# Kernel optimization log

Hardware: AMD Instinct MI355X
Metric: run time of the kernel (lower is better)

## Reference

```python
import jax, jax.numpy as jnp
import numpy as np

N = 30000      # nodes
E = 480000     # edges
NF = 92        # node features
EF = 50        # edge features
D1 = 64        # dim1
D2 = 64        # dim2
L = 3          # conv_count
FC = 2         # fc_count
G = 256        # graphs in batch
EPS = 1e-5


def setup_inputs() -> dict:
    key = jax.random.key(0)
    ks = jax.random.split(key, 20)
    s = 0.05
    zd = 2 * D1 + EF  # CGConv concat dim
    inp = {
        "x": jax.random.normal(ks[0], (N, NF), jnp.float32),
        "edge_attr": jax.random.uniform(ks[1], (E, EF), jnp.float32),
        "lin0_w": jax.random.normal(ks[2], (NF, D1), jnp.float32) * s,
        "lin0_b": jnp.zeros((D1,), jnp.float32),
        "conv_wf": jax.random.normal(ks[3], (L, zd, D1), jnp.float32) * s,
        "conv_bf": jnp.zeros((L, D1), jnp.float32),
        "conv_ws": jax.random.normal(ks[4], (L, zd, D1), jnp.float32) * s,
        "conv_bs": jnp.zeros((L, D1), jnp.float32),
        "bn_gamma": jnp.ones((L, D1), jnp.float32),
        "bn_beta": jnp.zeros((L, D1), jnp.float32),
        "lin1_w": jax.random.normal(ks[5], (D1, D2), jnp.float32) * s,
        "lin1_b": jnp.zeros((D2,), jnp.float32),
        "fc_w": jax.random.normal(ks[6], (FC, D2, D2), jnp.float32) * s,
        "fc_b": jnp.zeros((FC, D2), jnp.float32),
        "lin2_w": jax.random.normal(ks[7], (D2, 1), jnp.float32) * s,
        "lin2_b": jnp.zeros((1,), jnp.float32),
        "edge_index": jax.random.randint(ks[8], (2, E), 0, N),
        "batch": jnp.sort(jax.random.randint(ks[9], (N,), 0, G)),
        "n_graphs": G,
    }
    return inp


def reference(x, edge_attr, lin0_w, lin0_b, conv_wf, conv_bf, conv_ws, conv_bs,
              bn_gamma, bn_beta, lin1_w, lin1_b, fc_w, fc_b, lin2_w, lin2_b,
              edge_index, batch, n_graphs):
    n = x.shape[0]
    src = edge_index[0]  # x_j (source)
    dst = edge_index[1]  # x_i (target, aggregation index)
    h = jax.nn.relu(x @ lin0_w + lin0_b)  # [N, D1]

    # per-target edge counts for mean aggregation (constant across layers)
    cnt = jax.ops.segment_sum(jnp.ones((src.shape[0],), h.dtype), dst, num_segments=n)
    cnt = jnp.maximum(cnt, 1.0)[:, None]

    for l in range(L):
        # z = [x_i || x_j || e_ij]  -> gated message sigmoid(Wf z) * softplus(Ws z)
        z = jnp.concatenate([h[dst], h[src], edge_attr], axis=-1)  # [E, 2*D1+EF]
        m = jax.nn.sigmoid(z @ conv_wf[l] + conv_bf[l]) * jax.nn.softplus(z @ conv_ws[l] + conv_bs[l])
        aggr = jax.ops.segment_sum(m, dst, num_segments=n) / cnt  # mean aggr [N, D1]
        # BatchNorm (training-mode batch stats, biased variance as in torch)
        mu = jnp.mean(aggr, axis=0)
        var = jnp.var(aggr, axis=0)
        aggr = (aggr - mu) * jax.lax.rsqrt(var + EPS) * bn_gamma[l] + bn_beta[l]
        h = jax.nn.relu(h + aggr)  # residual then outer ReLU

    # global mean pool over graphs
    gcnt = jnp.maximum(jax.ops.segment_sum(jnp.ones((n,), h.dtype), batch, num_segments=n_graphs), 1.0)[:, None]
    out = jax.ops.segment_sum(h, batch, num_segments=n_graphs) / gcnt  # [G, D1]

    out = jax.nn.relu(out @ lin1_w + lin1_b)
    for f in range(FC):
        out = jax.nn.relu(out @ fc_w[f] + fc_b[f])
    out = out @ lin2_w + lin2_b
    return out.reshape(-1)  # [G]
```

## Files before the change

kernel.cpp:

```cpp
#include <hip/hip_runtime.h>
#include <hip/hip_bf16.h>

#define N_NODES 30000
#define N_EDGES 480000
#define NFEAT 92
#define EFEAT 50
#define D1 64
#define ZD 178
#define NL 3
#define NG 256
#define BN_EPS 1e-5f
#define NTILES (N_EDGES / 16)
#define EDGE_BLOCKS 7500
#define EDGE_GRID 7504

#define LIN0_BLOCKS 512
#define CNT_BLOCKS 1875
#define WPREP_BLOCKS 96
#define SCAN_BLOCKS ((N_NODES + 255) / 256)
#define BUILD_BLOCKS 1875
#define NP_BLOCKS 1024

typedef __attribute__((ext_vector_type(8))) short bf16x8;
typedef __attribute__((ext_vector_type(8))) unsigned short u16x8;
typedef __attribute__((ext_vector_type(4))) unsigned short u16x4;
typedef __attribute__((ext_vector_type(4))) float f32x4;

static __device__ __forceinline__ unsigned short f2bf(float v) {
  __hip_bfloat16 b = __float2bfloat16(v);
  return *(unsigned short*)&b;
}
static __device__ __forceinline__ float bfu(unsigned short u) {
  union { unsigned int i; float f; } c;
  c.i = ((unsigned int)u) << 16;
  return c.f;
}

static __device__ __forceinline__ void nodeproj_body(
    int blk0, int nblk, const float* __restrict__ hin, float* __restrict__ hout,
    const float* __restrict__ wfp, const float* __restrict__ wsm,
    unsigned short* __restrict__ projd_pk, unsigned short* __restrict__ projs_pk,
    const float* __restrict__ aggr, float* __restrict__ aggr_z,
    const float* __restrict__ invc, const float* __restrict__ musum,
    const float* __restrict__ sqsum, const float* __restrict__ gamma,
    const float* __restrict__ beta, int do_bn, float (*hl)[64]) {
  const int lane = threadIdx.x & 63;
  const int w = threadIdx.x >> 6;
  const float* W = (w < 2) ? wfp : wsm;
  const int roff = (w & 1) * 64;
  float wreg[D1];
#pragma unroll
  for (int k = 0; k < D1; ++k) wreg[k] = W[(size_t)(roff + k) * D1 + lane];
  unsigned short* pk = (w & 1) ? projs_pk : projd_pk;
  const int slot = (w < 2) ? 0 : 4;
  const int poff = (lane >> 2) * 8 + (lane & 3) + slot;
  float r = 0.0f, sh = 0.0f;
  if (do_bn) {
    const float mu = musum[lane] * (1.0f / N_NODES);
    const float var = sqsum[lane] * (1.0f / N_NODES) - mu * mu;
    r = gamma[lane] * rsqrtf(var + BN_EPS);
    sh = beta[lane] - mu * r;
  }
  for (int i = blk0; i < N_NODES; i += nblk) {
    float hv = hin[(size_t)i * D1 + lane];
    if (do_bn) {
      const float av = aggr[(size_t)i * D1 + lane] * invc[i];
      hv = fmaxf(hv + fmaf(av, r, sh), 0.0f);
      if (w == 0) hout[(size_t)i * D1 + lane] = hv;
    }
    if (w == 1) aggr_z[(size_t)i * D1 + lane] = 0.0f;
    hl[w][lane] = hv;
    __builtin_amdgcn_wave_barrier();
    const float4* hr = (const float4*)&hl[w][0];
    float acc = 0.0f;
#pragma unroll
    for (int k4 = 0; k4 < D1 / 4; ++k4) {
      const float4 v = hr[k4];
      acc = fmaf(v.x, wreg[4 * k4 + 0], acc);
      acc = fmaf(v.y, wreg[4 * k4 + 1], acc);
      acc = fmaf(v.z, wreg[4 * k4 + 2], acc);
      acc = fmaf(v.w, wreg[4 * k4 + 3], acc);
    }
    pk[(size_t)i * 128 + poff] = f2bf(acc);
    __builtin_amdgcn_wave_barrier();
  }
}

extern "C" __global__ void __launch_bounds__(256)
k_init(const float* __restrict__ x, const float* __restrict__ w,
       const float* __restrict__ b, float* __restrict__ h,
       const int* __restrict__ ei, int* __restrict__ cnt,
       const float* __restrict__ conv_wf, const float* __restrict__ conv_ws,
       unsigned short* __restrict__ Bp) {
  const int blk = blockIdx.x;
  if (blk < LIN0_BLOCKS) {
    const int lane = threadIdx.x & 63;
    const int wave = (blk * 256 + threadIdx.x) >> 6;
    const int nw = (LIN0_BLOCKS * 256) >> 6;
    float wreg[NFEAT];
#pragma unroll
    for (int k = 0; k < NFEAT; ++k) wreg[k] = w[k * D1 + lane];
    const float bj = b[lane];
    for (int i = wave; i < N_NODES; i += nw) {
      const float2* xr = (const float2*)(x + (size_t)i * NFEAT);
      float acc = bj;
#pragma unroll
      for (int k = 0; k < NFEAT / 2; ++k) {
        const float2 v = xr[k];
        acc = fmaf(v.x, wreg[2 * k], acc);
        acc = fmaf(v.y, wreg[2 * k + 1], acc);
      }
      h[(size_t)i * D1 + lane] = fmaxf(acc, 0.0f);
    }
  } else if (blk < LIN0_BLOCKS + CNT_BLOCKS) {
    const int e = (blk - LIN0_BLOCKS) * 256 + threadIdx.x;
    if (e < N_EDGES) atomicAdd(&cnt[ei[N_EDGES + e]], 1);
  } else {
    const int idx = (blk - LIN0_BLOCKS - CNT_BLOCKS) * 256 + threadIdx.x;
    const int j = idx & 7;
    const int lane = (idx >> 3) & 63;
    const int frag = (idx >> 9) & 15;
    const int l = idx >> 13;
    const int n = frag & 3;
    const int t = (frag >> 2) & 1;
    const int m = frag >> 3;
    const int k = t * 32 + (lane >> 4) * 8 + j;
    const int feat = (lane & 15) * 4 + n;
    float v = 0.0f;
    if (k < EFEAT) {
      const float* W = (m == 0) ? conv_wf : conv_ws;
      v = W[(size_t)l * ZD * D1 + (size_t)(128 + k) * D1 + feat];
    }
    Bp[idx] = f2bf(v);
  }
}

extern "C" __global__ void __launch_bounds__(256)
k_scan1(const int* __restrict__ cnt, int* __restrict__ lpre, int* __restrict__ ptot) {
  const int t = threadIdx.x;
  const int idx = blockIdx.x * 256 + t;
  const int v = (idx < N_NODES) ? cnt[idx] : 0;
  __shared__ int bs[256];
  bs[t] = v;
  __syncthreads();
  for (int off = 1; off < 256; off <<= 1) {
    int u = (t >= off) ? bs[t - off] : 0;
    __syncthreads();
    bs[t] += u;
    __syncthreads();
  }
  if (idx < N_NODES) lpre[idx] = bs[t] - v;
  if (t == 255) ptot[blockIdx.x] = bs[255];
}

extern "C" __global__ void __launch_bounds__(256)
k_scan23(const int* __restrict__ cnt, const int* __restrict__ lpre,
         const int* __restrict__ ptot, const int* __restrict__ batch,
         int* __restrict__ wptr, float* __restrict__ invc,
         int* __restrict__ grp) {
  __shared__ int bs[128];
  const int t = threadIdx.x;
  if (t < 128) bs[t] = (t < SCAN_BLOCKS) ? ptot[t] : 0;
  __syncthreads();
  for (int off = 1; off < 128; off <<= 1) {
    int u = 0;
    if (t < 128 && t >= off) u = bs[t - off];
    __syncthreads();
    if (t < 128 && t >= off) bs[t] += u;
    __syncthreads();
  }
  const int idx = blockIdx.x * 256 + t;
  if (idx >= N_NODES) return;
  const int bid = idx >> 8;
  const int boff = (bid == 0) ? 0 : bs[bid - 1];
  wptr[idx] = boff + lpre[idx];
  invc[idx] = 1.0f / fmaxf((float)cnt[idx], 1.0f);
  const int bt = batch[idx];
  if (idx == 0)
    for (int g = 0; g <= bt; ++g) grp[g] = 0;
  else {
    const int pb = batch[idx - 1];
    for (int g = pb + 1; g <= bt; ++g) grp[g] = idx;
  }
  if (idx == N_NODES - 1)
    for (int g = bt + 1; g <= NG; ++g) grp[g] = N_NODES;
}

extern "C" __global__ void __launch_bounds__(256)
k_build(const int* __restrict__ ei, int* __restrict__ wptr,
        int2* __restrict__ ds2, const float* __restrict__ ea,
        unsigned short* __restrict__ eapb,
        const float* __restrict__ h0, const float* __restrict__ wfl,
        const float* __restrict__ wsl, unsigned short* __restrict__ projd_pk,
        unsigned short* __restrict__ projs_pk, float* __restrict__ aggrA) {
  __shared__ __align__(16) int lpos[256];
  if (blockIdx.x >= BUILD_BLOCKS) {
    nodeproj_body(blockIdx.x - BUILD_BLOCKS, NP_BLOCKS, h0, nullptr, wfl, wsl,
                  projd_pk, projs_pk, nullptr, aggrA, nullptr, nullptr, nullptr,
                  nullptr, nullptr, 0, (float(*)[64])lpos);
    return;
  }
  const int e0 = blockIdx.x * 256;
  {
    const int e = e0 + threadIdx.x;
    const int d = ei[N_EDGES + e];
    const int pos = atomicAdd(&wptr[d], 1);
    ds2[pos] = make_int2(d, ei[e]);
    lpos[threadIdx.x] = pos;
  }
  __syncthreads();
  const int l16 = threadIdx.x & 15;
  const int sub = threadIdx.x >> 4;
#pragma unroll
  for (int r = 0; r < 16; ++r) {
    const int eb = r * 16 + sub;
    const size_t ge = e0 + eb;
    const int pos = lpos[eb];
    unsigned short o0 = 0, o1 = 0, o2 = 0, o3 = 0;
    if (l16 < 12) {
      const float4 v = *(const float4*)(ea + ge * EFEAT + l16 * 4);
      o0 = f2bf(v.x); o1 = f2bf(v.y); o2 = f2bf(v.z); o3 = f2bf(v.w);
    } else if (l16 == 12) {
      const float2 v = *(const float2*)(ea + ge * EFEAT + 48);
      o0 = f2bf(v.x); o1 = f2bf(v.y);
    }
    u16x4 st;
    st[0] = o0; st[1] = o1; st[2] = o2; st[3] = o3;
    *(u16x4*)(eapb + ((size_t)pos << 6) + l16 * 4) = st;
  }
}

extern "C" __global__ void __launch_bounds__(256)
k_nodeproj(const float* __restrict__ hin, float* __restrict__ hout,
           const float* __restrict__ wfp, const float* __restrict__ wsm,
           unsigned short* __restrict__ projd_pk, unsigned short* __restrict__ projs_pk,
           const float* __restrict__ aggr, float* __restrict__ aggr_z,
           const float* __restrict__ invc,
           const float* __restrict__ musum, const float* __restrict__ sqsum,
           const float* __restrict__ gamma, const float* __restrict__ beta) {
  __shared__ float hl[4][64];
  nodeproj_body(blockIdx.x, gridDim.x, hin, hout, wfp, wsm, projd_pk, projs_pk,
                aggr, aggr_z, invc, musum, sqsum, gamma, beta, 1, hl);
}

extern "C" __global__ void __launch_bounds__(256)
k_edgemm(const unsigned short* __restrict__ projd_pk,
         const unsigned short* __restrict__ projs_pk,
         const unsigned short* __restrict__ eapb,
         const int2* __restrict__ ds2,
         const unsigned short* __restrict__ Bp,
         const float* __restrict__ bfp, const float* __restrict__ bsp,
         float* __restrict__ aggr, float* __restrict__ musum,
         float* __restrict__ sqsum) {
  const int lane = threadIdx.x & 63;
  const int wv = threadIdx.x >> 6;
  const int col = lane & 15;
  const int quad = lane >> 4;
  __shared__ float mlds[4][16][68];

  const int vbid = (blockIdx.x & 7) * 938 + (blockIdx.x >> 3);
  if (blockIdx.x == 0 && wv == 0) {
    musum[lane] = 0.0f;
    sqsum[lane] = 0.0f;
  }
  if (vbid >= EDGE_BLOCKS) return;

  const int t = vbid * 4 + wv;
  const int base = t * 16;

  const int4 p01 = *(const int4*)(ds2 + base + quad * 4);
  const int4 p23 = *(const int4*)(ds2 + base + quad * 4 + 2);
  const int dr[4] = {p01.x, p01.z, p23.x, p23.z};
  const int sr[4] = {p01.y, p01.w, p23.y, p23.w};
  const bf16x8 Af0 = *(const bf16x8*)(eapb + ((size_t)(base + col) << 6) + quad * 8);
  const bf16x8 Af1 = *(const bf16x8*)(eapb + ((size_t)(base + col) << 6) + 32 + quad * 8);

  bf16x8 Bf[2][2][4];
#pragma unroll
  for (int m = 0; m < 2; ++m)
#pragma unroll
    for (int tt = 0; tt < 2; ++tt)
#pragma unroll
      for (int n = 0; n < 4; ++n)
        Bf[m][tt][n] = *(const bf16x8*)(Bp + ((((m * 2 + tt) * 4 + n) * 64 + lane) * 8));

  const f32x4 bf4 = *(const f32x4*)(bfp + col * 4);
  const f32x4 bs4 = *(const f32x4*)(bsp + col * 4);

  f32x4 aF[4], aS[4];
#pragma unroll
  for (int r = 0; r < 4; ++r) {
    const int d = dr[r];
    const int s = sr[r];
    const u16x8 pd = *(const u16x8*)(projd_pk + (size_t)d * 128 + col * 8);
    const u16x8 ss = *(const u16x8*)(projs_pk + (size_t)s * 128 + col * 8);
#pragma unroll
    for (int n = 0; n < 4; ++n) {
      aF[n][r] = bfu(pd[n]) + bfu(ss[n]) + bf4[n];
      aS[n][r] = bfu(pd[n + 4]) + bfu(ss[n + 4]) + bs4[n];
    }
  }

#pragma unroll
  for (int n = 0; n < 4; ++n) {
    aF[n] = __builtin_amdgcn_mfma_f32_16x16x32_bf16(Af0, Bf[0][0][n], aF[n], 0, 0, 0);
    aF[n] = __builtin_amdgcn_mfma_f32_16x16x32_bf16(Af1, Bf[0][1][n], aF[n], 0, 0, 0);
    aS[n] = __builtin_amdgcn_mfma_f32_16x16x32_bf16(Af0, Bf[1][0][n], aS[n], 0, 0, 0);
    aS[n] = __builtin_amdgcn_mfma_f32_16x16x32_bf16(Af1, Bf[1][1][n], aS[n], 0, 0, 0);
  }

#pragma unroll
  for (int r = 0; r < 4; ++r) {
    f32x4 mv;
#pragma unroll
    for (int n = 0; n < 4; ++n) {
      const float af = aF[n][r];
      const float as = aS[n][r];
      const float sg = __builtin_amdgcn_rcpf(1.0f + __expf(-af));
      const float sp = fmaxf(as, 0.0f) + __logf(1.0f + __expf(-fabsf(as)));
      mv[n] = sg * sp;
    }
    *(f32x4*)&mlds[wv][quad * 4 + r][col * 4] = mv;
  }
  __builtin_amdgcn_wave_barrier();

  float sum = 0.0f;
  int dcur = ds2[base].x;
#pragma unroll
  for (int p = 0; p < 16; ++p) {
    sum += mlds[wv][p][lane];
    const int dnxt = (p < 15) ? ds2[base + p + 1].x : -1;
    if (dnxt != dcur) {
      atomicAdd(&aggr[(size_t)dcur * D1 + lane], sum);
      sum = 0.0f;
      dcur = dnxt;
    }
  }
}

extern "C" __global__ void __launch_bounds__(256)
k_stats(const float* __restrict__ aggr, const float* __restrict__ invc,
        float* __restrict__ musum, float* __restrict__ sqsum) {
  const int j = threadIdx.x & 63;
  const int rid = (blockIdx.x * blockDim.x + threadIdx.x) >> 6;
  const int rstr = (gridDim.x * blockDim.x) >> 6;
  float s = 0.0f, sq = 0.0f;
  for (int i = rid; i < N_NODES; i += rstr) {
    const float v = aggr[(size_t)i * D1 + j] * invc[i];
    s += v;
    sq = fmaf(v, v, sq);
  }
  __shared__ float ls[256], lq[256];
  ls[threadIdx.x] = s;
  lq[threadIdx.x] = sq;
  __syncthreads();
  if (threadIdx.x < 64) {
    s = ls[j] + ls[64 + j] + ls[128 + j] + ls[192 + j];
    sq = lq[j] + lq[64 + j] + lq[128 + j] + lq[192 + j];
    atomicAdd(&musum[j], s);
    atomicAdd(&sqsum[j], sq);
  }
}

extern "C" __global__ void __launch_bounds__(256)
k_poolmlp(const float* __restrict__ h, const float* __restrict__ aggr,
          const float* __restrict__ invc,
          const float* __restrict__ musum, const float* __restrict__ sqsum,
          const float* __restrict__ gamma, const float* __restrict__ beta,
          const int* __restrict__ grp,
          const float* __restrict__ lin1_w, const float* __restrict__ lin1_b,
          const float* __restrict__ fc_w, const float* __restrict__ fc_b,
          const float* __restrict__ lin2_w, const float* __restrict__ lin2_b,
          float* __restrict__ out) {
  const int g = blockIdx.x;
  const int lane = threadIdx.x & 63;
  const int wv = threadIdx.x >> 6;
  const float mu = musum[lane] * (1.0f / N_NODES);
  const float var = sqsum[lane] * (1.0f / N_NODES) - mu * mu;
  const float r = gamma[lane] * rsqrtf(var + BN_EPS);
  const float sh = beta[lane] - mu * r;
  const int s = grp[g], e = grp[g + 1];
  float acc = 0.0f;
  for (int i = s + wv; i < e; i += 4) {
    const float hv = h[(size_t)i * D1 + lane];
    const float av = aggr[(size_t)i * D1 + lane] * invc[i];
    acc += fmaxf(hv + fmaf(av, r, sh), 0.0f);
  }
  __shared__ float red[4][64];
  __shared__ float vin[64];
  red[wv][lane] = acc;
  __syncthreads();
  const int j = threadIdx.x;
  float v = 0.0f;
  if (j < 64) {
    const float inv = 1.0f / fmaxf((float)(e - s), 1.0f);
    v = (red[0][j] + red[1][j] + red[2][j] + red[3][j]) * inv;
  }
  for (int layer = 0; layer < 3; ++layer) {
    if (j < 64) vin[j] = v;
    __syncthreads();
    if (j < 64) {
      const float* W;
      const float* B;
      if (layer == 0) {
        W = lin1_w;
        B = lin1_b;
      } else {
        W = fc_w + (size_t)(layer - 1) * D1 * D1;
        B = fc_b + (size_t)(layer - 1) * D1;
      }
      float a2 = B[j];
#pragma unroll 16
      for (int k = 0; k < D1; ++k) a2 = fmaf(vin[k], W[k * D1 + j], a2);
      v = fmaxf(a2, 0.0f);
    }
    __syncthreads();
  }
  if (j < 64) {
    float p = v * lin2_w[j];
#pragma unroll
    for (int off = 32; off > 0; off >>= 1) p += __shfl_down(p, off);
    if (j == 0) out[g] = p + lin2_b[0];
  }
}

extern "C" void kernel_launch(void* const* d_in, const int* in_sizes, int n_in,
                              void* d_out, int out_size, void* d_ws, size_t ws_size,
                              hipStream_t stream) {
  const float* x        = (const float*)d_in[0];
  const float* ea       = (const float*)d_in[1];
  const float* lin0_w   = (const float*)d_in[2];
  const float* lin0_b   = (const float*)d_in[3];
  const float* conv_wf  = (const float*)d_in[4];
  const float* conv_bf  = (const float*)d_in[5];
  const float* conv_ws  = (const float*)d_in[6];
  const float* conv_bs  = (const float*)d_in[7];
  const float* bn_gamma = (const float*)d_in[8];
  const float* bn_beta  = (const float*)d_in[9];
  const float* lin1_w   = (const float*)d_in[10];
  const float* lin1_b   = (const float*)d_in[11];
  const float* fc_w     = (const float*)d_in[12];
  const float* fc_b     = (const float*)d_in[13];
  const float* lin2_w   = (const float*)d_in[14];
  const float* lin2_b   = (const float*)d_in[15];
  const int*   ei       = (const int*)d_in[16];
  const int*   batch    = (const int*)d_in[17];

  uintptr_t p = (uintptr_t)d_ws;
  auto alloc = [&](size_t bytes) {
    p = (p + 255) & ~(size_t)255;
    void* r = (void*)p;
    p += bytes;
    return r;
  };
  float* h0     = (float*)alloc((size_t)N_NODES * 64 * 4);
  float* h1     = (float*)alloc((size_t)N_NODES * 64 * 4);
  unsigned short* projd_pk = (unsigned short*)alloc((size_t)N_NODES * 128 * 2);
  unsigned short* projs_pk = (unsigned short*)alloc((size_t)N_NODES * 128 * 2);
  float* aggrA  = (float*)alloc((size_t)N_NODES * 64 * 4);
  float* aggrB  = (float*)alloc((size_t)N_NODES * 64 * 4);
  float* musum  = (float*)alloc(128 * 4);
  float* sqsum  = musum + 64;
  float* invc   = (float*)alloc((size_t)N_NODES * 4);
  int*   cnt    = (int*)alloc((size_t)N_NODES * 4);
  int*   lpre   = (int*)alloc((size_t)N_NODES * 4);
  int*   ptot   = (int*)alloc((size_t)SCAN_BLOCKS * 4);
  int*   wptr   = (int*)alloc((size_t)N_NODES * 4);
  int2*  ds2    = (int2*)alloc((size_t)N_EDGES * 8);
  int*   grp    = (int*)alloc((size_t)(NG + 1) * 4);
  unsigned short* eapb = (unsigned short*)alloc((size_t)N_EDGES * 64 * 2);
  unsigned short* Bp   = (unsigned short*)alloc((size_t)NL * 16 * 64 * 8 * 2);

  hipMemsetAsync(cnt, 0, N_NODES * sizeof(int), stream);
  k_init<<<LIN0_BLOCKS + CNT_BLOCKS + WPREP_BLOCKS, 256, 0, stream>>>(
      x, lin0_w, lin0_b, h0, ei, cnt, conv_wf, conv_ws, Bp);
  k_scan1<<<SCAN_BLOCKS, 256, 0, stream>>>(cnt, lpre, ptot);
  k_scan23<<<SCAN_BLOCKS, 256, 0, stream>>>(cnt, lpre, ptot, batch, wptr, invc, grp);
  k_build<<<BUILD_BLOCKS + NP_BLOCKS, 256, 0, stream>>>(
      ei, wptr, ds2, ea, eapb, h0, conv_wf, conv_ws, projd_pk, projs_pk, aggrA);

  float* aggr_of[NL] = {aggrA, aggrB, aggrA};
  const float* hin_of[NL]  = {h0, h0, h1};
  float* hout_of[NL]       = {h0, h1, h0};

  for (int l = 0; l < NL; ++l) {
    const float* wfl = conv_wf + (size_t)l * ZD * D1;
    const float* wsl = conv_ws + (size_t)l * ZD * D1;
    if (l > 0)
      k_nodeproj<<<1024, 256, 0, stream>>>(
          hin_of[l], hout_of[l], wfl, wsl, projd_pk, projs_pk,
          aggr_of[l - 1], aggr_of[l], invc, musum, sqsum,
          bn_gamma + (size_t)(l - 1) * D1, bn_beta + (size_t)(l - 1) * D1);
    k_edgemm<<<EDGE_GRID, 256, 0, stream>>>(
        projd_pk, projs_pk, eapb, ds2,
        Bp + (size_t)l * 16 * 64 * 8,
        conv_bf + (size_t)l * D1, conv_bs + (size_t)l * D1,
        aggr_of[l], musum, sqsum);
    k_stats<<<256, 256, 0, stream>>>(aggr_of[l], invc, musum, sqsum);
  }

  k_poolmlp<<<NG, 256, 0, stream>>>(h0, aggr_of[2], invc, musum, sqsum,
                                    bn_gamma + (size_t)2 * D1, bn_beta + (size_t)2 * D1,
                                    grp, lin1_w, lin1_b, fc_w, fc_b,
                                    lin2_w, lin2_b, (float*)d_out);
}
```

Before: 621.7 us.

## Fuse whole pipeline into one cooperative persistent kernel with grid syncs

Replaces the sequence of separate kernel launches (init, scans, build, per-layer nodeproj/edge/stats, pool) with a single cooperative kernel of 1024 persistent blocks. The phases are separated by grid.sync, and the edge loop is grid-strided instead of one tile per block. Per-layer BN statistics now get separate buffers and are zeroed up front. This removes launch gaps and tail effects between the many small kernels. The cost is grid-wide barrier overhead, lower occupancy from __launch_bounds__(256,4) and fewer blocks on the edge phase. A fallback multi-kernel path is kept for devices without cooperative launch.

```diff
diff --git a/kernel.cpp b/kernel.cpp
--- a/kernel.cpp
+++ b/kernel.cpp
@@ -1,5 +1,8 @@
 #include <hip/hip_runtime.h>
 #include <hip/hip_bf16.h>
+#include <hip/hip_cooperative_groups.h>
+
+namespace cg = cooperative_groups;
 
 #define N_NODES 30000
 #define N_EDGES 480000
@@ -11,20 +14,25 @@
 #define NG 256
 #define BN_EPS 1e-5f
 #define NTILES (N_EDGES / 16)
-#define EDGE_BLOCKS 7500
-#define EDGE_GRID 7504
-
-#define LIN0_BLOCKS 512
-#define CNT_BLOCKS 1875
-#define WPREP_BLOCKS 96
 #define SCAN_BLOCKS ((N_NODES + 255) / 256)
-#define BUILD_BLOCKS 1875
-#define NP_BLOCKS 1024
+#define BUILD_CHUNKS 1875
+#define NB 1024
+#define SMEM_BYTES 17408
 
 typedef __attribute__((ext_vector_type(8))) short bf16x8;
 typedef __attribute__((ext_vector_type(8))) unsigned short u16x8;
 typedef __attribute__((ext_vector_type(4))) unsigned short u16x4;
 typedef __attribute__((ext_vector_type(4))) float f32x4;
+
+struct KParams {
+  const float *x, *ea, *lin0_w, *lin0_b, *conv_wf, *conv_bf, *conv_ws, *conv_bs;
+  const float *bn_gamma, *bn_beta, *lin1_w, *lin1_b, *fc_w, *fc_b, *lin2_w, *lin2_b;
+  const int *ei, *batch;
+  float *h0, *h1, *aggrA, *aggrB, *stat, *invc, *out;
+  unsigned short *projd, *projs, *eapb, *Bp;
+  int *cnt, *lpre, *ptot, *wptr, *grp;
+  int2 *ds2;
+};
 
 static __device__ __forceinline__ unsigned short f2bf(float v) {
   __hip_bfloat16 b = __float2bfloat16(v);
@@ -68,7 +76,7 @@
       hv = fmaxf(hv + fmaf(av, r, sh), 0.0f);
       if (w == 0) hout[(size_t)i * D1 + lane] = hv;
     }
-    if (w == 1) aggr_z[(size_t)i * D1 + lane] = 0.0f;
+    if (w == 1 && aggr_z) aggr_z[(size_t)i * D1 + lane] = 0.0f;
     hl[w][lane] = hv;
     __builtin_amdgcn_wave_barrier();
     const float4* hr = (const float4*)&hl[w][0];
@@ -86,23 +94,18 @@
   }
 }
 
-extern "C" __global__ void __launch_bounds__(256)
-k_init(const float* __restrict__ x, const float* __restrict__ w,
-       const float* __restrict__ b, float* __restrict__ h,
-       const int* __restrict__ ei, int* __restrict__ cnt,
-       const float* __restrict__ conv_wf, const float* __restrict__ conv_ws,
-       unsigned short* __restrict__ Bp) {
-  const int blk = blockIdx.x;
-  if (blk < LIN0_BLOCKS) {
-    const int lane = threadIdx.x & 63;
-    const int wave = (blk * 256 + threadIdx.x) >> 6;
-    const int nw = (LIN0_BLOCKS * 256) >> 6;
+static __device__ void phase0(const KParams& p) {
+  const int tid = threadIdx.x, bid = blockIdx.x;
+  const int lane = tid & 63, wv = tid >> 6;
+  const int gw = bid * 4 + wv, nw = gridDim.x * 4;
+  const int gt = bid * 256 + tid, nt = gridDim.x * 256;
+  {
     float wreg[NFEAT];
 #pragma unroll
-    for (int k = 0; k < NFEAT; ++k) wreg[k] = w[k * D1 + lane];
-    const float bj = b[lane];
-    for (int i = wave; i < N_NODES; i += nw) {
-      const float2* xr = (const float2*)(x + (size_t)i * NFEAT);
+    for (int k = 0; k < NFEAT; ++k) wreg[k] = p.lin0_w[k * D1 + lane];
+    const float bj = p.lin0_b[lane];
+    for (int i = gw; i < N_NODES; i += nw) {
+      const float2* xr = (const float2*)(p.x + (size_t)i * NFEAT);
       float acc = bj;
 #pragma unroll
       for (int k = 0; k < NFEAT / 2; ++k) {
@@ -110,37 +113,38 @@
         acc = fmaf(v.x, wreg[2 * k], acc);
         acc = fmaf(v.y, wreg[2 * k + 1], acc);
       }
-      h[(size_t)i * D1 + lane] = fmaxf(acc, 0.0f);
-    }
-  } else if (blk < LIN0_BLOCKS + CNT_BLOCKS) {
-    const int e = (blk - LIN0_BLOCKS) * 256 + threadIdx.x;
-    if (e < N_EDGES) atomicAdd(&cnt[ei[N_EDGES + e]], 1);
-  } else {
-    const int idx = (blk - LIN0_BLOCKS - CNT_BLOCKS) * 256 + threadIdx.x;
+      p.h0[(size_t)i * D1 + lane] = fmaxf(acc, 0.0f);
+    }
+  }
+  for (int e = gt; e < N_EDGES; e += nt) atomicAdd(&p.cnt[p.ei[N_EDGES + e]], 1);
+  for (int idx = gt; idx < NL * 16 * 64 * 8; idx += nt) {
     const int j = idx & 7;
-    const int lane = (idx >> 3) & 63;
+    const int ln = (idx >> 3) & 63;
     const int frag = (idx >> 9) & 15;
     const int l = idx >> 13;
     const int n = frag & 3;
     const int t = (frag >> 2) & 1;
     const int m = frag >> 3;
-    const int k = t * 32 + (lane >> 4) * 8 + j;
-    const int feat = (lane & 15) * 4 + n;
+    const int k = t * 32 + (ln >> 4) * 8 + j;
+    const int feat = (ln & 15) * 4 + n;
     float v = 0.0f;
     if (k < EFEAT) {
-      const float* W = (m == 0) ? conv_wf : conv_ws;
+      const float* W = (m == 0) ? p.conv_wf : p.conv_ws;
       v = W[(size_t)l * ZD * D1 + (size_t)(128 + k) * D1 + feat];
     }
-    Bp[idx] = f2bf(v);
-  }
-}
-
-extern "C" __global__ void __launch_bounds__(256)
-k_scan1(const int* __restrict__ cnt, int* __restrict__ lpre, int* __restrict__ ptot) {
+    p.Bp[idx] = f2bf(v);
+  }
+  for (int i = gt; i < N_NODES * D1; i += nt) p.aggrA[i] = 0.0f;
+  if (bid == 0 && tid < NL * 128) p.stat[tid] = 0.0f;
+}
+
+static __device__ void phase_scan1(const KParams& p, char* smem) {
+  const int bid = blockIdx.x;
+  if (bid >= SCAN_BLOCKS) return;
+  int* bs = (int*)smem;
   const int t = threadIdx.x;
-  const int idx = blockIdx.x * 256 + t;
-  const int v = (idx < N_NODES) ? cnt[idx] : 0;
-  __shared__ int bs[256];
+  const int idx = bid * 256 + t;
+  const int v = (idx < N_NODES) ? p.cnt[idx] : 0;
   bs[t] = v;
   __syncthreads();
   for (int off = 1; off < 256; off <<= 1) {
@@ -149,18 +153,16 @@
     bs[t] += u;
     __syncthreads();
   }
-  if (idx < N_NODES) lpre[idx] = bs[t] - v;
-  if (t == 255) ptot[blockIdx.x] = bs[255];
-}
-
-extern "C" __global__ void __launch_bounds__(256)
-k_scan23(const int* __restrict__ cnt, const int* __restrict__ lpre,
-         const int* __restrict__ ptot, const int* __restrict__ batch,
-         int* __restrict__ wptr, float* __restrict__ invc,
-         int* __restrict__ grp) {
-  __shared__ int bs[128];
+  if (idx < N_NODES) p.lpre[idx] = bs[t] - v;
+  if (t == 255) p.ptot[bid] = bs[255];
+}
+
+static __device__ void phase_scan23(const KParams& p, char* smem) {
+  const int bid = blockIdx.x;
+  if (bid >= SCAN_BLOCKS) return;
+  int* bs = (int*)smem;
   const int t = threadIdx.x;
-  if (t < 128) bs[t] = (t < SCAN_BLOCKS) ? ptot[t] : 0;
+  if (t < 128) bs[t] = (t < SCAN_BLOCKS) ? p.ptot[t] : 0;
   __syncthreads();
   for (int off = 1; off < 128; off <<= 1) {
     int u = 0;
@@ -169,225 +171,200 @@
     if (t < 128 && t >= off) bs[t] += u;
     __syncthreads();
   }
-  const int idx = blockIdx.x * 256 + t;
+  const int idx = bid * 256 + t;
   if (idx >= N_NODES) return;
-  const int bid = idx >> 8;
-  const int boff = (bid == 0) ? 0 : bs[bid - 1];
-  wptr[idx] = boff + lpre[idx];
-  invc[idx] = 1.0f / fmaxf((float)cnt[idx], 1.0f);
-  const int bt = batch[idx];
+  const int bb = idx >> 8;
+  const int boff = (bb == 0) ? 0 : bs[bb - 1];
+  p.wptr[idx] = boff + p.lpre[idx];
+  p.invc[idx] = 1.0f / fmaxf((float)p.cnt[idx], 1.0f);
+  const int bt = p.batch[idx];
   if (idx == 0)
-    for (int g = 0; g <= bt; ++g) grp[g] = 0;
+    for (int g = 0; g <= bt; ++g) p.grp[g] = 0;
   else {
-    const int pb = batch[idx - 1];
-    for (int g = pb + 1; g <= bt; ++g) grp[g] = idx;
+    const int pb = p.batch[idx - 1];
+    for (int g = pb + 1; g <= bt; ++g) p.grp[g] = idx;
   }
   if (idx == N_NODES - 1)
-    for (int g = bt + 1; g <= NG; ++g) grp[g] = N_NODES;
-}
-
-extern "C" __global__ void __launch_bounds__(256)
-k_build(const int* __restrict__ ei, int* __restrict__ wptr,
-        int2* __restrict__ ds2, const float* __restrict__ ea,
-        unsigned short* __restrict__ eapb,
-        const float* __restrict__ h0, const float* __restrict__ wfl,
-        const float* __restrict__ wsl, unsigned short* __restrict__ projd_pk,
-        unsigned short* __restrict__ projs_pk, float* __restrict__ aggrA) {
-  __shared__ __align__(16) int lpos[256];
-  if (blockIdx.x >= BUILD_BLOCKS) {
-    nodeproj_body(blockIdx.x - BUILD_BLOCKS, NP_BLOCKS, h0, nullptr, wfl, wsl,
-                  projd_pk, projs_pk, nullptr, aggrA, nullptr, nullptr, nullptr,
-                  nullptr, nullptr, 0, (float(*)[64])lpos);
-    return;
-  }
-  const int e0 = blockIdx.x * 256;
-  {
-    const int e = e0 + threadIdx.x;
-    const int d = ei[N_EDGES + e];
-    const int pos = atomicAdd(&wptr[d], 1);
-    ds2[pos] = make_int2(d, ei[e]);
-    lpos[threadIdx.x] = pos;
-  }
+    for (int g = bt + 1; g <= NG; ++g) p.grp[g] = N_NODES;
+}
+
+static __device__ void phase3(const KParams& p, char* smem) {
+  int* lpos = (int*)smem;
+  float (*hl)[64] = (float(*)[64])(smem + 1024);
+  const int tid = threadIdx.x, bid = blockIdx.x;
+  for (int c = bid; c < BUILD_CHUNKS; c += gridDim.x) {
+    const int e0 = c * 256;
+    {
+      const int e = e0 + tid;
+      const int d = p.ei[N_EDGES + e];
+      const int pos = atomicAdd(&p.wptr[d], 1);
+      p.ds2[pos] = make_int2(d, p.ei[e]);
+      lpos[tid] = pos;
+    }
+    __syncthreads();
+    const int l16 = tid & 15;
+    const int sub = tid >> 4;
+#pragma unroll
+    for (int r = 0; r < 16; ++r) {
+      const int eb = r * 16 + sub;
+      const size_t ge = e0 + eb;
+      const int pos = lpos[eb];
+      unsigned short o0 = 0, o1 = 0, o2 = 0, o3 = 0;
+      if (l16 < 12) {
+        const float4 v = *(const float4*)(p.ea + ge * EFEAT + l16 * 4);
+        o0 = f2bf(v.x); o1 = f2bf(v.y); o2 = f2bf(v.z); o3 = f2bf(v.w);
+      } else if (l16 == 12) {
+        const float2 v = *(const float2*)(p.ea + ge * EFEAT + 48);
+        o0 = f2bf(v.x); o1 = f2bf(v.y);
+      }
+      u16x4 st;
+      st[0] = o0; st[1] = o1; st[2] = o2; st[3] = o3;
+      *(u16x4*)(p.eapb + ((size_t)pos << 6) + l16 * 4) = st;
+    }
+    __syncthreads();
+  }
+  nodeproj_body(bid, gridDim.x, p.h0, nullptr, p.conv_wf, p.conv_ws, p.projd, p.projs,
+                nullptr, nullptr, nullptr, nullptr, nullptr, nullptr, nullptr, 0, hl);
+}
+
+static __device__ void phase_edge(const KParams& p, int l, char* smem) {
+  float (*mlds)[16][68] = (float(*)[16][68])smem;
+  const int tid = threadIdx.x, bid = blockIdx.x;
+  const int lane = tid & 63, wv = tid >> 6;
+  const int col = lane & 15, quad = lane >> 4;
+  const unsigned short* Bpl = p.Bp + (size_t)l * 16 * 64 * 8;
+  const float* bfp = p.conv_bf + (size_t)l * D1;
+  const float* bsp = p.conv_bs + (size_t)l * D1;
+  float* aggr = (l == 1) ? p.aggrB : p.aggrA;
+
+  bf16x8 Bf[2][2][4];
+#pragma unroll
+  for (int m = 0; m < 2; ++m)
+#pragma unroll
+    for (int tt = 0; tt < 2; ++tt)
+#pragma unroll
+      for (int n = 0; n < 4; ++n)
+        Bf[m][tt][n] = *(const bf16x8*)(Bpl + ((((m * 2 + tt) * 4 + n) * 64 + lane) * 8));
+  const f32x4 bf4 = *(const f32x4*)(bfp + col * 4);
+  const f32x4 bs4 = *(const f32x4*)(bsp + col * 4);
+
+  const int gw = bid * 4 + wv, nw = gridDim.x * 4;
+  for (int t = gw; t < NTILES; t += nw) {
+    const int base = t * 16;
+    const int4 p01 = *(const int4*)(p.ds2 + base + quad * 4);
+    const int4 p23 = *(const int4*)(p.ds2 + base + quad * 4 + 2);
+    const int dr[4] = {p01.x, p01.z, p23.x, p23.z};
+    const int sr[4] = {p01.y, p01.w, p23.y, p23.w};
+    const bf16x8 Af0 = *(const bf16x8*)(p.eapb + ((size_t)(base + col) << 6) + quad * 8);
+    const bf16x8 Af1 = *(const bf16x8*)(p.eapb + ((size_t)(base + col) << 6) + 32 + quad * 8);
+
+    f32x4 aF[4], aS[4];
+#pragma unroll
+    for (int r = 0; r < 4; ++r) {
+      const u16x8 pd = *(const u16x8*)(p.projd + (size_t)dr[r] * 128 + col * 8);
+      const u16x8 ss = *(const u16x8*)(p.projs + (size_t)sr[r] * 128 + col * 8);
+#pragma unroll
+      for (int n = 0; n < 4; ++n) {
+        aF[n][r] = bfu(pd[n]) + bfu(ss[n]) + bf4[n];
+        aS[n][r] = bfu(pd[n + 4]) + bfu(ss[n + 4]) + bs4[n];
+      }
+    }
+#pragma unroll
+    for (int n = 0; n < 4; ++n) {
+      aF[n] = __builtin_amdgcn_mfma_f32_16x16x32_bf16(Af0, Bf[0][0][n], aF[n], 0, 0, 0);
+      aF[n] = __builtin_amdgcn_mfma_f32_16x16x32_bf16(Af1, Bf[0][1][n], aF[n], 0, 0, 0);
+      aS[n] = __builtin_amdgcn_mfma_f32_16x16x32_bf16(Af0, Bf[1][0][n], aS[n], 0, 0, 0);
+      aS[n] = __builtin_amdgcn_mfma_f32_16x16x32_bf16(Af1, Bf[1][1][n], aS[n], 0, 0, 0);
+    }
+#pragma unroll
+    for (int r = 0; r < 4; ++r) {
+      f32x4 mv;
+#pragma unroll
+      for (int n = 0; n < 4; ++n) {
+        const float af = aF[n][r];
+        const float as = aS[n][r];
+        const float sg = __builtin_amdgcn_rcpf(1.0f + __expf(-af));
+        const float sp = fmaxf(as, 0.0f) + __logf(1.0f + __expf(-fabsf(as)));
+        mv[n] = sg * sp;
+      }
+      *(f32x4*)&mlds[wv][quad * 4 + r][col * 4] = mv;
+    }
+    __builtin_amdgcn_wave_barrier();
+    float sum = 0.0f;
+    int dcur = p.ds2[base].x;
+#pragma unroll
+    for (int q = 0; q < 16; ++q) {
+      sum += mlds[wv][q][lane];
+      const int dnxt = (q < 15) ? p.ds2[base + q + 1].x : -1;
+      if (dnxt != dcur) {
+        atomicAdd(&aggr[(size_t)dcur * D1 + lane], sum);
+        sum = 0.0f;
+        dcur = dnxt;
+      }
+    }
+    __builtin_amdgcn_wave_barrier();
+  }
+}
+
+static __device__ void phase_stats(const KParams& p, int l, char* smem) {
+  float* ls = (float*)smem;
+  float* lq = ls + 256;
+  const int tid = threadIdx.x, bid = blockIdx.x;
+  const int j = tid & 63;
+  const float* aggr = (l == 1) ? p.aggrB : p.aggrA;
+  float* st = p.stat + (size_t)l * 128;
+  const int rid = bid * 4 + (tid >> 6);
+  const int rstr = gridDim.x * 4;
+  float s = 0.0f, sq = 0.0f;
+  for (int i = rid; i < N_NODES; i += rstr) {
+    const float v = aggr[(size_t)i * D1 + j] * p.invc[i];
+    s += v;
+    sq = fmaf(v, v, sq);
+  }
+  ls[tid] = s;
+  lq[tid] = sq;
   __syncthreads();
-  const int l16 = threadIdx.x & 15;
-  const int sub = threadIdx.x >> 4;
-#pragma unroll
-  for (int r = 0; r < 16; ++r) {
-    const int eb = r * 16 + sub;
-    const size_t ge = e0 + eb;
-    const int pos = lpos[eb];
-    unsigned short o0 = 0, o1 = 0, o2 = 0, o3 = 0;
-    if (l16 < 12) {
-      const float4 v = *(const float4*)(ea + ge * EFEAT + l16 * 4);
-      o0 = f2bf(v.x); o1 = f2bf(v.y); o2 = f2bf(v.z); o3 = f2bf(v.w);
-    } else if (l16 == 12) {
-      const float2 v = *(const float2*)(ea + ge * EFEAT + 48);
-      o0 = f2bf(v.x); o1 = f2bf(v.y);
-    }
-    u16x4 st;
-    st[0] = o0; st[1] = o1; st[2] = o2; st[3] = o3;
-    *(u16x4*)(eapb + ((size_t)pos << 6) + l16 * 4) = st;
-  }
-}
-
-extern "C" __global__ void __launch_bounds__(256)
-k_nodeproj(const float* __restrict__ hin, float* __restrict__ hout,
-           const float* __restrict__ wfp, const float* __restrict__ wsm,
-           unsigned short* __restrict__ projd_pk, unsigned short* __restrict__ projs_pk,
-           const float* __restrict__ aggr, float* __restrict__ aggr_z,
-           const float* __restrict__ invc,
-           const float* __restrict__ musum, const float* __restrict__ sqsum,
-           const float* __restrict__ gamma, const float* __restrict__ beta) {
-  __shared__ float hl[4][64];
-  nodeproj_body(blockIdx.x, gridDim.x, hin, hout, wfp, wsm, projd_pk, projs_pk,
-                aggr, aggr_z, invc, musum, sqsum, gamma, beta, 1, hl);
-}
-
-extern "C" __global__ void __launch_bounds__(256)
-k_edgemm(const unsigned short* __restrict__ projd_pk,
-         const unsigned short* __restrict__ projs_pk,
-         const unsigned short* __restrict__ eapb,
-         const int2* __restrict__ ds2,
-         const unsigned short* __restrict__ Bp,
-         const float* __restrict__ bfp, const float* __restrict__ bsp,
-         float* __restrict__ aggr, float* __restrict__ musum,
-         float* __restrict__ sqsum) {
+  if (tid < 64) {
+    s = ls[j] + ls[64 + j] + ls[128 + j] + ls[192 + j];
+    sq = lq[j] + lq[64 + j] + lq[128 + j] + lq[192 + j];
+    atomicAdd(&st[j], s);
+    atomicAdd(&st[64 + j], sq);
+  }
+  __syncthreads();
+}
+
+static __device__ void phase_np(const KParams& p, int l, char* smem) {
+  float (*hl)[64] = (float(*)[64])smem;
+  const float* ag = (l == 1) ? p.aggrB : p.aggrA;
+  float* agz = (l == 0) ? p.aggrB : p.aggrA;
+  const float* hin = (l == 0) ? p.h0 : p.h1;
+  float* hout = (l == 0) ? p.h1 : p.h0;
+  nodeproj_body(blockIdx.x, gridDim.x, hin, hout,
+                p.conv_wf + (size_t)(l + 1) * ZD * D1, p.conv_ws + (size_t)(l + 1) * ZD * D1,
+                p.projd, p.projs, ag, agz, p.invc,
+                p.stat + (size_t)l * 128, p.stat + (size_t)l * 128 + 64,
+                p.bn_gamma + (size_t)l * D1, p.bn_beta + (size_t)l * D1, 1, hl);
+}
+
+static __device__ void phase_pool(const KParams& p, char* smem) {
+  const int g = blockIdx.x;
+  if (g >= NG) return;
+  float (*red)[64] = (float(*)[64])smem;
+  float* vin = (float*)(smem + 1024);
   const int lane = threadIdx.x & 63;
   const int wv = threadIdx.x >> 6;
-  const int col = lane & 15;
-  const int quad = lane >> 4;
-  __shared__ float mlds[4][16][68];
-
-  const int vbid = (blockIdx.x & 7) * 938 + (blockIdx.x >> 3);
-  if (blockIdx.x == 0 && wv == 0) {
-    musum[lane] = 0.0f;
-    sqsum[lane] = 0.0f;
-  }
-  if (vbid >= EDGE_BLOCKS) return;
-
-  const int t = vbid * 4 + wv;
-  const int base = t * 16;
-
-  const int4 p01 = *(const int4*)(ds2 + base + quad * 4);
-  const int4 p23 = *(const int4*)(ds2 + base + quad * 4 + 2);
-  const int dr[4] = {p01.x, p01.z, p23.x, p23.z};
-  const int sr[4] = {p01.y, p01.w, p23.y, p23.w};
-  const bf16x8 Af0 = *(const bf16x8*)(eapb + ((size_t)(base + col) << 6) + quad * 8);
-  const bf16x8 Af1 = *(const bf16x8*)(eapb + ((size_t)(base + col) << 6) + 32 + quad * 8);
-
-  bf16x8 Bf[2][2][4];
-#pragma unroll
-  for (int m = 0; m < 2; ++m)
-#pragma unroll
-    for (int tt = 0; tt < 2; ++tt)
-#pragma unroll
-      for (int n = 0; n < 4; ++n)
-        Bf[m][tt][n] = *(const bf16x8*)(Bp + ((((m * 2 + tt) * 4 + n) * 64 + lane) * 8));
-
-  const f32x4 bf4 = *(const f32x4*)(bfp + col * 4);
-  const f32x4 bs4 = *(const f32x4*)(bsp + col * 4);
-
-  f32x4 aF[4], aS[4];
-#pragma unroll
-  for (int r = 0; r < 4; ++r) {
-    const int d = dr[r];
-    const int s = sr[r];
-    const u16x8 pd = *(const u16x8*)(projd_pk + (size_t)d * 128 + col * 8);
-    const u16x8 ss = *(const u16x8*)(projs_pk + (size_t)s * 128 + col * 8);
-#pragma unroll
-    for (int n = 0; n < 4; ++n) {
-      aF[n][r] = bfu(pd[n]) + bfu(ss[n]) + bf4[n];
-      aS[n][r] = bfu(pd[n + 4]) + bfu(ss[n + 4]) + bs4[n];
-    }
-  }
-
-#pragma unroll
-  for (int n = 0; n < 4; ++n) {
-    aF[n] = __builtin_amdgcn_mfma_f32_16x16x32_bf16(Af0, Bf[0][0][n], aF[n], 0, 0, 0);
-    aF[n] = __builtin_amdgcn_mfma_f32_16x16x32_bf16(Af1, Bf[0][1][n], aF[n], 0, 0, 0);
-    aS[n] = __builtin_amdgcn_mfma_f32_16x16x32_bf16(Af0, Bf[1][0][n], aS[n], 0, 0, 0);
-    aS[n] = __builtin_amdgcn_mfma_f32_16x16x32_bf16(Af1, Bf[1][1][n], aS[n], 0, 0, 0);
-  }
-
-#pragma unroll
-  for (int r = 0; r < 4; ++r) {
-    f32x4 mv;
-#pragma unroll
-    for (int n = 0; n < 4; ++n) {
-      const float af = aF[n][r];
-      const float as = aS[n][r];
-      const float sg = __builtin_amdgcn_rcpf(1.0f + __expf(-af));
-      const float sp = fmaxf(as, 0.0f) + __logf(1.0f + __expf(-fabsf(as)));
-      mv[n] = sg * sp;
-    }
-    *(f32x4*)&mlds[wv][quad * 4 + r][col * 4] = mv;
-  }
-  __builtin_amdgcn_wave_barrier();
-
-  float sum = 0.0f;
-  int dcur = ds2[base].x;
-#pragma unroll
-  for (int p = 0; p < 16; ++p) {
-    sum += mlds[wv][p][lane];
-    const int dnxt = (p < 15) ? ds2[base + p + 1].x : -1;
-    if (dnxt != dcur) {
-      atomicAdd(&aggr[(size_t)dcur * D1 + lane], sum);
-      sum = 0.0f;
-      dcur = dnxt;
-    }
-  }
-}
-
-extern "C" __global__ void __launch_bounds__(256)
-k_stats(const float* __restrict__ aggr, const float* __restrict__ invc,
-        float* __restrict__ musum, float* __restrict__ sqsum) {
-  const int j = threadIdx.x & 63;
-  const int rid = (blockIdx.x * blockDim.x + threadIdx.x) >> 6;
-  const int rstr = (gridDim.x * blockDim.x) >> 6;
-  float s = 0.0f, sq = 0.0f;
-  for (int i = rid; i < N_NODES; i += rstr) {
-    const float v = aggr[(size_t)i * D1 + j] * invc[i];
-    s += v;
-    sq = fmaf(v, v, sq);
-  }
-  __shared__ float ls[256], lq[256];
-  ls[threadIdx.x] = s;
-  lq[threadIdx.x] = sq;
-  __syncthreads();
-  if (threadIdx.x < 64) {
-    s = ls[j] + ls[64 + j] + ls[128 + j] + ls[192 + j];
-    sq = lq[j] + lq[64 + j] + lq[128 + j] + lq[192 + j];
-    atomicAdd(&musum[j], s);
-    atomicAdd(&sqsum[j], sq);
-  }
-}
-
-extern "C" __global__ void __launch_bounds__(256)
-k_poolmlp(const float* __restrict__ h, const float* __restrict__ aggr,
-          const float* __restrict__ invc,
-          const float* __restrict__ musum, const float* __restrict__ sqsum,
-          const float* __restrict__ gamma, const float* __restrict__ beta,
-          const int* __restrict__ grp,
-          const float* __restrict__ lin1_w, const float* __restrict__ lin1_b,
-          const float* __restrict__ fc_w, const float* __restrict__ fc_b,
-          const float* __restrict__ lin2_w, const float* __restrict__ lin2_b,
-          float* __restrict__ out) {
-  const int g = blockIdx.x;
-  const int lane = threadIdx.x & 63;
-  const int wv = threadIdx.x >> 6;
-  const float mu = musum[lane] * (1.0f / N_NODES);
-  const float var = sqsum[lane] * (1.0f / N_NODES) - mu * mu;
-  const float r = gamma[lane] * rsqrtf(var + BN_EPS);
-  const float sh = beta[lane] - mu * r;
-  const int s = grp[g], e = grp[g + 1];
+  const float* st = p.stat + 2 * 128;
+  const float mu = st[lane] * (1.0f / N_NODES);
+  const float var = st[64 + lane] * (1.0f / N_NODES) - mu * mu;
+  const float r = p.bn_gamma[2 * D1 + lane] * rsqrtf(var + BN_EPS);
+  const float sh = p.bn_beta[2 * D1 + lane] - mu * r;
+  const int s = p.grp[g], e = p.grp[g + 1];
   float acc = 0.0f;
   for (int i = s + wv; i < e; i += 4) {
-    const float hv = h[(size_t)i * D1 + lane];
-    const float av = aggr[(size_t)i * D1 + lane] * invc[i];
+    const float hv = p.h0[(size_t)i * D1 + lane];
+    const float av = p.aggrA[(size_t)i * D1 + lane] * p.invc[i];
     acc += fmaxf(hv + fmaf(av, r, sh), 0.0f);
   }
-  __shared__ float red[4][64];
-  __shared__ float vin[64];
   red[wv][lane] = acc;
   __syncthreads();
   const int j = threadIdx.x;
@@ -402,13 +379,8 @@
     if (j < 64) {
       const float* W;
       const float* B;
-      if (layer == 0) {
-        W = lin1_w;
-        B = lin1_b;
-      } else {
-        W = fc_w + (size_t)(layer - 1) * D1 * D1;
-        B = fc_b + (size_t)(layer - 1) * D1;
-      }
+      if (layer == 0) { W = p.lin1_w; B = p.lin1_b; }
+      else { W = p.fc_w + (size_t)(layer - 1) * D1 * D1; B = p.fc_b + (size_t)(layer - 1) * D1; }
       float a2 = B[j];
 #pragma unroll 16
       for (int k = 0; k < D1; ++k) a2 = fmaf(vin[k], W[k * D1 + j], a2);
@@ -417,90 +389,121 @@
     __syncthreads();
   }
   if (j < 64) {
-    float p = v * lin2_w[j];
-#pragma unroll
-    for (int off = 32; off > 0; off >>= 1) p += __shfl_down(p, off);
-    if (j == 0) out[g] = p + lin2_b[0];
-  }
+    float pr = v * p.lin2_w[j];
+#pragma unroll
+    for (int off = 32; off > 0; off >>= 1) pr += __shfl_down(pr, off);
+    if (j == 0) p.out[g] = pr + p.lin2_b[0];
+  }
+}
+
+__global__ void __launch_bounds__(256, 4) k_mega(KParams p) {
+  __shared__ __align__(16) char smem[SMEM_BYTES];
+  cg::grid_group grid = cg::this_grid();
+  phase0(p);                 grid.sync();
+  phase_scan1(p, smem);      grid.sync();
+  phase_scan23(p, smem);     grid.sync();
+  phase3(p, smem);           grid.sync();
+  for (int l = 0; l < NL; ++l) {
+    phase_edge(p, l, smem);  grid.sync();
+    phase_stats(p, l, smem); grid.sync();
+    if (l < NL - 1) { phase_np(p, l, smem); grid.sync(); }
+  }
+  phase_pool(p, smem);
+}
+
+__global__ void __launch_bounds__(256) k_w0(KParams p) { phase0(p); }
+__global__ void __launch_bounds__(256) k_ws1(KParams p) {
+  __shared__ __align__(16) char smem[SMEM_BYTES]; phase_scan1(p, smem);
+}
+__global__ void __launch_bounds__(256) k_ws2(KParams p) {
+  __shared__ __align__(16) char smem[SMEM_BYTES]; phase_scan23(p, smem);
+}
+__global__ void __launch_bounds__(256) k_w3(KParams p) {
+  __shared__ __align__(16) char smem[SMEM_BYTES]; phase3(p, smem);
+}
+__global__ void __launch_bounds__(256) k_we(KParams p, int l) {
+  __shared__ __align__(16) char smem[SMEM_BYTES]; phase_edge(p, l, smem);
+}
+__global__ void __launch_bounds__(256) k_wst(KParams p, int l) {
+  __shared__ __align__(16) char smem[SMEM_BYTES]; phase_stats(p, l, smem);
+}
+__global__ void __launch_bounds__(256) k_wnp(KParams p, int l) {
+  __shared__ __align__(16) char smem[SMEM_BYTES]; phase_np(p, l, smem);
+}
+__global__ void __launch_bounds__(256) k_wpool(KParams p) {
+  __shared__ __align__(16) char smem[SMEM_BYTES]; phase_pool(p, smem);
 }
 
 extern "C" void kernel_launch(void* const* d_in, const int* in_sizes, int n_in,
                               void* d_out, int out_size, void* d_ws, size_t ws_size,
                               hipStream_t stream) {
-  const float* x        = (const float*)d_in[0];
-  const float* ea       = (const float*)d_in[1];
-  const float* lin0_w   = (const float*)d_in[2];
-  const float* lin0_b   = (const float*)d_in[3];
-  const float* conv_wf  = (const float*)d_in[4];
-  const float* conv_bf  = (const float*)d_in[5];
-  const float* conv_ws  = (const float*)d_in[6];
-  const float* conv_bs  = (const float*)d_in[7];
-  const float* bn_gamma = (const float*)d_in[8];
-  const float* bn_beta  = (const float*)d_in[9];
-  const float* lin1_w   = (const float*)d_in[10];
-  const float* lin1_b   = (const float*)d_in[11];
-  const float* fc_w     = (const float*)d_in[12];
-  const float* fc_b     = (const float*)d_in[13];
-  const float* lin2_w   = (const float*)d_in[14];
-  const float* lin2_b   = (const float*)d_in[15];
-  const int*   ei       = (const int*)d_in[16];
-  const int*   batch    = (const int*)d_in[17];
-
-  uintptr_t p = (uintptr_t)d_ws;
+  KParams P;
+  P.x        = (const float*)d_in[0];
+  P.ea       = (const float*)d_in[1];
+  P.lin0_w   = (const float*)d_in[2];
+  P.lin0_b   = (const float*)d_in[3];
+  P.conv_wf  = (const float*)d_in[4];
+  P.conv_bf  = (const float*)d_in[5];
+  P.conv_ws  = (const float*)d_in[6];
+  P.conv_bs  = (const float*)d_in[7];
+  P.bn_gamma = (const float*)d_in[8];
+  P.bn_beta  = (const float*)d_in[9];
+  P.lin1_w   = (const float*)d_in[10];
+  P.lin1_b   = (const float*)d_in[11];
+  P.fc_w     = (const float*)d_in[12];
+  P.fc_b     = (const float*)d_in[13];
+  P.lin2_w   = (const float*)d_in[14];
+  P.lin2_b   = (const float*)d_in[15];
+  P.ei       = (const int*)d_in[16];
+  P.batch    = (const int*)d_in[17];
+  P.out      = (float*)d_out;
+
+  uintptr_t pp = (uintptr_t)d_ws;
   auto alloc = [&](size_t bytes) {
-    p = (p + 255) & ~(size_t)255;
-    void* r = (void*)p;
-    p += bytes;
+    pp = (pp + 255) & ~(size_t)255;
+    void* r = (void*)pp;
+    pp += bytes;
     return r;
   };
-  float* h0     = (float*)alloc((size_t)N_NODES * 64 * 4);
-  float* h1     = (float*)alloc((size_t)N_NODES * 64 * 4);
-  unsigned short* projd_pk = (unsigned short*)alloc((size_t)N_NODES * 128 * 2);
-  unsigned short* projs_pk = (unsigned short*)alloc((size_t)N_NODES * 128 * 2);
-  float* aggrA  = (float*)alloc((size_t)N_NODES * 64 * 4);
-  float* aggrB  = (float*)alloc((size_t)N_NODES * 64 * 4);
-  float* musum  = (float*)alloc(128 * 4);
-  float* sqsum  = musum + 64;
-  float* invc   = (float*)alloc((size_t)N_NODES * 4);
-  int*   cnt    = (int*)alloc((size_t)N_NODES * 4);
-  int*   lpre   = (int*)alloc((size_t)N_NODES * 4);
-  int*   ptot   = (int*)alloc((size_t)SCAN_BLOCKS * 4);
-  int*   wptr   = (int*)alloc((size_t)N_NODES * 4);
-  int2*  ds2    = (int2*)alloc((size_t)N_EDGES * 8);
-  int*   grp    = (int*)alloc((size_t)(NG + 1) * 4);
-  unsigned short* eapb = (unsigned short*)alloc((size_t)N_EDGES * 64 * 2);
-  unsigned short* Bp   = (unsigned short*)alloc((size_t)NL * 16 * 64 * 8 * 2);
-
-  hipMemsetAsync(cnt, 0, N_NODES * sizeof(int), stream);
-  k_init<<<LIN0_BLOCKS + CNT_BLOCKS + WPREP_BLOCKS, 256, 0, stream>>>(
-      x, lin0_w, lin0_b, h0, ei, cnt, conv_wf, conv_ws, Bp);
-  k_scan1<<<SCAN_BLOCKS, 256, 0, stream>>>(cnt, lpre, ptot);
-  k_scan23<<<SCAN_BLOCKS, 256, 0, stream>>>(cnt, lpre, ptot, batch, wptr, invc, grp);
-  k_build<<<BUILD_BLOCKS + NP_BLOCKS, 256, 0, stream>>>(
-      ei, wptr, ds2, ea, eapb, h0, conv_wf, conv_ws, projd_pk, projs_pk, aggrA);
-
-  float* aggr_of[NL] = {aggrA, aggrB, aggrA};
-  const float* hin_of[NL]  = {h0, h0, h1};
-  float* hout_of[NL]       = {h0, h1, h0};
-
+  P.h0    = (float*)alloc((size_t)N_NODES * 64 * 4);
+  P.h1    = (float*)alloc((size_t)N_NODES * 64 * 4);
+  P.projd = (unsigned short*)alloc((size_t)N_NODES * 128 * 2);
+  P.projs = (unsigned short*)alloc((size_t)N_NODES * 128 * 2);
+  P.aggrA = (float*)alloc((size_t)N_NODES * 64 * 4);
+  P.aggrB = (float*)alloc((size_t)N_NODES * 64 * 4);
+  P.stat  = (float*)alloc((size_t)NL * 128 * 4);
+  P.invc  = (float*)alloc((size_t)N_NODES * 4);
+  P.cnt   = (int*)alloc((size_t)N_NODES * 4);
+  P.lpre  = (int*)alloc((size_t)N_NODES * 4);
+  P.ptot  = (int*)alloc((size_t)SCAN_BLOCKS * 4);
+  P.wptr  = (int*)alloc((size_t)N_NODES * 4);
+  P.ds2   = (int2*)alloc((size_t)N_EDGES * 8);
+  P.grp   = (int*)alloc((size_t)(NG + 1) * 4);
+  P.eapb  = (unsigned short*)alloc((size_t)N_EDGES * 64 * 2);
+  P.Bp    = (unsigned short*)alloc((size_t)NL * 16 * 64 * 8 * 2);
+
+  hipMemsetAsync(P.cnt, 0, N_NODES * sizeof(int), stream);
+
+  int dev = 0;
+  (void)hipGetDevice(&dev);
+  int coop = 0;
+  (void)hipDeviceGetAttribute(&coop, hipDeviceAttributeCooperativeLaunch, dev);
+  if (coop) {
+    void* kargs[] = {(void*)&P};
+    hipError_t err = hipLaunchCooperativeKernel((const void*)k_mega, dim3(NB), dim3(256),
+                                                kargs, 0, stream);
+    if (err == hipSuccess) return;
+    (void)hipGetLastError();
+  }
+
+  k_w0<<<NB, 256, 0, stream>>>(P);
+  k_ws1<<<SCAN_BLOCKS, 256, 0, stream>>>(P);
+  k_ws2<<<SCAN_BLOCKS, 256, 0, stream>>>(P);
+  k_w3<<<NB, 256, 0, stream>>>(P);
   for (int l = 0; l < NL; ++l) {
-    const float* wfl = conv_wf + (size_t)l * ZD * D1;
-    const float* wsl = conv_ws + (size_t)l * ZD * D1;
-    if (l > 0)
-      k_nodeproj<<<1024, 256, 0, stream>>>(
-          hin_of[l], hout_of[l], wfl, wsl, projd_pk, projs_pk,
-          aggr_of[l - 1], aggr_of[l], invc, musum, sqsum,
-          bn_gamma + (size_t)(l - 1) * D1, bn_beta + (size_t)(l - 1) * D1);
-    k_edgemm<<<EDGE_GRID, 256, 0, stream>>>(
-        projd_pk, projs_pk, eapb, ds2,
-        Bp + (size_t)l * 16 * 64 * 8,
-        conv_bf + (size_t)l * D1, conv_bs + (size_t)l * D1,
-        aggr_of[l], musum, sqsum);
-    k_stats<<<256, 256, 0, stream>>>(aggr_of[l], invc, musum, sqsum);
-  }
-
-  k_poolmlp<<<NG, 256, 0, stream>>>(h0, aggr_of[2], invc, musum, sqsum,
-                                    bn_gamma + (size_t)2 * D1, bn_beta + (size_t)2 * D1,
-                                    grp, lin1_w, lin1_b, fc_w, fc_b,
-                                    lin2_w, lin2_b, (float*)d_out);
-}
+    k_we<<<NB, 256, 0, stream>>>(P, l);
+    k_wst<<<NB, 256, 0, stream>>>(P, l);
+    if (l < NL - 1) k_wnp<<<NB, 256, 0, stream>>>(P, l);
+  }
+  k_wpool<<<NG, 256, 0, stream>>>(P);
+}
```

Result: slower. 2.115 ms (+240.2%).
